# Kernel optimization log

Measured on AMD Instinct MI355X. Metric: run time of the kernel, lower is better.

Reference implementation:

```python
import jax, jax.numpy as jnp
import numpy as np

DIM = 1024
N_HEADS = 16
HEAD_DIM = DIM // N_HEADS
B, T = 2, 2048


def setup_inputs() -> dict:
    key = jax.random.key(0)
    ks = jax.random.split(key, 6)
    x = jax.random.normal(ks[0], (B, T, DIM), dtype=jnp.float32)
    # causal 0/1 mask, broadcastable over batch and heads
    mask = jnp.tril(jnp.ones((T, T), dtype=jnp.int32))[None, None, :, :]
    s = 1.0 / np.sqrt(DIM)
    W_qkv = jax.random.normal(ks[1], (DIM, 3 * DIM), dtype=jnp.float32) * s
    b_qkv = jnp.zeros((3 * DIM,), dtype=jnp.float32)
    W_proj = jax.random.normal(ks[2], (DIM, DIM), dtype=jnp.float32) * s
    b_proj = jnp.zeros((DIM,), dtype=jnp.float32)
    return {"x": x, "W_qkv": W_qkv, "b_qkv": b_qkv, "W_proj": W_proj, "b_proj": b_proj, "mask": mask}


def reference(x, W_qkv, b_qkv, W_proj, b_proj, mask):
    Bx, Tx, C = x.shape
    qkv = x @ W_qkv + b_qkv  # [B,T,3C]
    q, k, v = jnp.split(qkv, 3, axis=-1)
    # [B,T,C] -> [B,H,T,Dh]
    def split_heads(t):
        return t.reshape(Bx, Tx, N_HEADS, HEAD_DIM).transpose(0, 2, 1, 3)
    q, k, v = split_heads(q), split_heads(k), split_heads(v)
    att = jnp.einsum('bhqd,bhkd->bhqk', q, k) / jnp.sqrt(jnp.float32(HEAD_DIM))
    att = jnp.where(mask == 0, jnp.float32(-jnp.inf), att)
    att = jax.nn.softmax(att, axis=-1)
    # dropout is identity in eval mode
    out = jnp.einsum('bhqk,bhkd->bhqd', att, v)
    out = out.transpose(0, 2, 1, 3).reshape(Bx, Tx, C)
    return out @ W_proj + b_proj
```

## Files before the change

### kernel.cpp

```cpp
#include <hip/hip_runtime.h>
#include <hip/hip_bf16.h>
#include <stdint.h>

#define DIM   1024
#define NHEAD 16
#define HD    64
#define SEQ   2048
#define NTOK  4096
#define QKV_REGION (NTOK * DIM)

typedef short          bf16x8 __attribute__((ext_vector_type(8)));
typedef float          f32x4  __attribute__((ext_vector_type(4)));
typedef float          f32x16 __attribute__((ext_vector_type(16)));
typedef unsigned short u16x8  __attribute__((ext_vector_type(8)));
typedef unsigned short u16x4  __attribute__((ext_vector_type(4)));

__device__ __forceinline__ unsigned short f2bf(float f) {
  union { float f; unsigned u; } x; x.f = f;
  unsigned r = x.u + 0x7FFFu + ((x.u >> 16) & 1u);
  return (unsigned short)(r >> 16);
}

__device__ __forceinline__ unsigned pack2bf_tr(float a, float b) {
  union { float f; unsigned u; } x, y; x.f = a; y.f = b;
  return (x.u >> 16) | (y.u & 0xFFFF0000u);
}

__device__ __forceinline__ void gld16(void* lds, const void* g) {
  __builtin_amdgcn_global_load_lds(
      (const __attribute__((address_space(1))) unsigned int*)g,
      (__attribute__((address_space(3))) unsigned int*)lds, 16, 0, 0);
}

__global__ __launch_bounds__(256) void k_prep(const float* __restrict__ x,
                                              unsigned short* __restrict__ xb,
                                              const float* __restrict__ Wqkv,
                                              unsigned short* __restrict__ wqkvt,
                                              const float* __restrict__ Wproj,
                                              unsigned short* __restrict__ wprojt) {
  __shared__ unsigned short t[64][72];
  const int bid = blockIdx.x, tid = threadIdx.x;
  if (bid < 2048) {
    size_t i = ((size_t)bid * 256 + tid) * 8;
    float4 a = *(const float4*)(x + i);
    float4 b = *(const float4*)(x + i + 4);
    u16x8 o;
    o[0] = f2bf(a.x); o[1] = f2bf(a.y); o[2] = f2bf(a.z); o[3] = f2bf(a.w);
    o[4] = f2bf(b.x); o[5] = f2bf(b.y); o[6] = f2bf(b.z); o[7] = f2bf(b.w);
    *(u16x8*)(xb + i) = o;
    return;
  }
  const float* in; unsigned short* out; int C, bx, by;
  if (bid < 2816) { in = Wqkv; out = wqkvt; C = 3072; bx = (bid - 2048) % 48; by = (bid - 2048) / 48; }
  else            { in = Wproj; out = wprojt; C = 1024; bx = (bid - 2816) % 16; by = (bid - 2816) / 16; }
  const int R = 1024;
  int r0 = by * 64, c0 = bx * 64;
  int rr = tid >> 4, cc = (tid & 15) * 4;
#pragma unroll
  for (int p = 0; p < 4; p++) {
    int r = p * 16 + rr;
    float4 v = *(const float4*)(in + (size_t)(r0 + r) * C + c0 + cc);
    t[r][cc + 0] = f2bf(v.x); t[r][cc + 1] = f2bf(v.y);
    t[r][cc + 2] = f2bf(v.z); t[r][cc + 3] = f2bf(v.w);
  }
  __syncthreads();
#pragma unroll
  for (int p = 0; p < 4; p++) {
    int c = p * 16 + rr;
    u16x4 v;
    v[0] = t[cc + 0][c]; v[1] = t[cc + 1][c];
    v[2] = t[cc + 2][c]; v[3] = t[cc + 3][c];
    *(u16x4*)(out + (size_t)(c0 + c) * R + r0 + cc) = v;
  }
}

__global__ __launch_bounds__(256) void k_tr_v(const unsigned short* __restrict__ v,
                                              unsigned short* __restrict__ vt) {
  __shared__ unsigned short s[64][72];
  int bh = blockIdx.y, t0 = blockIdx.x * 64;
  const unsigned short* in = v + (size_t)bh * SEQ * HD + (size_t)t0 * HD;
  unsigned short* out = vt + (size_t)bh * HD * SEQ + t0;
  int tid = threadIdx.x;
  int rr = tid >> 3, cc = (tid & 7) * 8;
#pragma unroll
  for (int p = 0; p < 2; p++) {
    int r = p * 32 + rr;
    u16x8 x = *(const u16x8*)(in + r * HD + cc);
#pragma unroll
    for (int j = 0; j < 8; j++) s[r][cc + j] = x[j];
  }
  __syncthreads();
#pragma unroll
  for (int p = 0; p < 2; p++) {
    int d = p * 32 + rr;
    u16x8 o;
#pragma unroll
    for (int j = 0; j < 8; j++) o[j] = s[cc + j][d];
    *(u16x8*)(out + (size_t)d * SEQ + cc) = o;
  }
}

template <int EPI>
__global__ __launch_bounds__(256) void k_gemm_bt(const unsigned short* __restrict__ A,
                                                 const unsigned short* __restrict__ Bt,
                                                 const float* __restrict__ bias,
                                                 void* __restrict__ Cout,
                                                 int M, int N, int K) {
  __shared__ unsigned short Al[128 * 64];
  __shared__ unsigned short Bl[128 * 64];
  const int tid = threadIdx.x, lane = tid & 63, w = tid >> 6;
  const int wm = w >> 1, wn = w & 1;
  const int m0 = blockIdx.y * 128, n0 = blockIdx.x * 128;
  const int l31 = lane & 31, hl = lane >> 5;

  f32x16 acc[2][2];
#pragma unroll
  for (int mt = 0; mt < 2; mt++)
#pragma unroll
    for (int nt = 0; nt < 2; nt++)
#pragma unroll
      for (int r = 0; r < 16; r++) acc[mt][nt][r] = 0.f;

  for (int k0 = 0; k0 < K; k0 += 64) {
    __syncthreads();
#pragma unroll
    for (int i = 0; i < 4; i++) {
      int row = w * 32 + i * 8 + (lane >> 3);
      int ch = (lane & 7) ^ (row & 7);
      gld16(&Al[(w * 32 + i * 8) * 64], A + (size_t)(m0 + row) * K + k0 + ch * 8);
      gld16(&Bl[(w * 32 + i * 8) * 64], Bt + (size_t)(n0 + row) * K + k0 + ch * 8);
    }
    __syncthreads();
#pragma unroll
    for (int ks = 0; ks < 4; ks++) {
      bf16x8 af[2], bfr[2];
#pragma unroll
      for (int mt = 0; mt < 2; mt++) {
        int row = wm * 64 + mt * 32 + l31;
        int ch = (2 * ks + hl) ^ (row & 7);
        af[mt] = *(const bf16x8*)&Al[row * 64 + ch * 8];
      }
#pragma unroll
      for (int nt = 0; nt < 2; nt++) {
        int row = wn * 64 + nt * 32 + l31;
        int ch = (2 * ks + hl) ^ (row & 7);
        bfr[nt] = *(const bf16x8*)&Bl[row * 64 + ch * 8];
      }
#pragma unroll
      for (int mt = 0; mt < 2; mt++)
#pragma unroll
        for (int nt = 0; nt < 2; nt++)
          acc[mt][nt] = __builtin_amdgcn_mfma_f32_32x32x16_bf16(af[mt], bfr[nt], acc[mt][nt], 0, 0, 0);
    }
  }

#pragma unroll
  for (int mt = 0; mt < 2; mt++) {
#pragma unroll
    for (int nt = 0; nt < 2; nt++) {
      int col = n0 + wn * 64 + nt * 32 + l31;
      float bv = bias[col];
#pragma unroll
      for (int rg = 0; rg < 4; rg++)
#pragma unroll
        for (int ri = 0; ri < 4; ri++) {
          int row = m0 + wm * 64 + mt * 32 + ri + rg * 8 + hl * 4;
          float val = acc[mt][nt][rg * 4 + ri] + bv;
          if (EPI == 1) {
            ((float*)Cout)[(size_t)row * N + col] = val;
          } else {
            unsigned short* dst = (unsigned short*)Cout;
            int reg = col >> 10, nn = col & 1023;
            if (reg == 0) val *= 0.18033688011112042f;
            int h = nn >> 6, d = nn & 63;
            int b = row >> 11, t = row & 2047;
            size_t idx = (size_t)reg * QKV_REGION +
                         ((size_t)(b * NHEAD + h) * SEQ + t) * HD + d;
            dst[idx] = f2bf(val);
          }
        }
    }
  }
}

__global__ __launch_bounds__(512, 4) void k_attn(const unsigned short* __restrict__ Q,
                                                 const unsigned short* __restrict__ K,
                                                 const unsigned short* __restrict__ Vt,
                                                 unsigned short* __restrict__ O) {
  __shared__ unsigned short kl[2][2][64 * 64];
  __shared__ unsigned short vl[2][2][64 * 64];
  __shared__ float ml2[256];
  const int tid = threadIdx.x, lane = tid & 63, w = tid >> 6;
  const int hl = lane >> 5, q32 = lane & 31;
  const bool hb = (hl != 0);
  const int h = w >> 2, wr = w & 3;
  const int id = blockIdx.x;
  const int bh = id & 31;
  const int qt = (id < 256) ? (15 - (id >> 5)) : ((id >> 5) - 8);
  const unsigned short* Qb = Q + (size_t)bh * SEQ * HD;
  const unsigned short* Kb = K + (size_t)bh * SEQ * HD;
  const unsigned short* Vb = Vt + (size_t)bh * HD * SEQ;

  const int wq = qt * 128 + wr * 32;
  const int qmax = wq + 31;
  const int qg = wq + q32;
  const int nlo = qt + 1;
  const int kt0 = h ? nlo : 0;

  bf16x8 qf[4];
  {
    const unsigned short* qp = Qb + (size_t)(wq + q32) * HD + hl * 8;
#pragma unroll
    for (int ks = 0; ks < 4; ks++) qf[ks] = *(const bf16x8*)(qp + ks * 16);
  }

  f32x16 oacc[2];
#pragma unroll
  for (int nd = 0; nd < 2; nd++)
#pragma unroll
    for (int r = 0; r < 16; r++) oacc[nd][r] = 0.f;
  float mrun = -1e30f, lpart = 0.f;

#define ASTAGE(S, BUF)                                                                   \
  if ((S) < nlo) {                                                                       \
    const int kb_ = (kt0 + (S)) * 64;                                                    \
    _Pragma("unroll")                                                                    \
    for (int i = 0; i < 2; i++) {                                                        \
      int row = wr * 16 + i * 8 + (lane >> 3);                                           \
      int ch = (lane & 7) ^ (row & 7);                                                   \
      gld16(&kl[h][BUF][(wr * 16 + i * 8) * 64], Kb + (size_t)(kb_ + row) * HD + ch * 8);\
      gld16(&vl[h][BUF][(wr * 16 + i * 8) * 64], Vb + (size_t)row * SEQ + kb_ + ch * 8); \
    }                                                                                    \
  }

  ASTAGE(0, 0);
  __syncthreads();
  int cur = 0;

  for (int s = 0; s < nlo; s++) {
    ASTAGE(s + 1, cur ^ 1);
    const int kb = (kt0 + s) * 64;
    if (kb <= qmax) {
      f32x16 sacc[2];
#pragma unroll
      for (int nk = 0; nk < 2; nk++)
#pragma unroll
        for (int r = 0; r < 16; r++) sacc[nk][r] = 0.f;
      __builtin_amdgcn_s_setprio(1);
#pragma unroll
      for (int ks = 0; ks < 4; ks++) {
#pragma unroll
        for (int nk = 0; nk < 2; nk++) {
          int krow = nk * 32 + q32;
          int ch = (2 * ks + hl) ^ (krow & 7);
          bf16x8 kf = *(const bf16x8*)&kl[h][cur][krow * 64 + ch * 8];
          sacc[nk] = __builtin_amdgcn_mfma_f32_32x32x16_bf16(kf, qf[ks], sacc[nk], 0, 0, 0);
        }
      }
      __builtin_amdgcn_s_setprio(0);

      const bool nm = (kb + 63 > wq);
      if (nm) {
        const int kvbase = kb + hl * 4;
#pragma unroll
        for (int nk = 0; nk < 2; nk++)
#pragma unroll
          for (int rg = 0; rg < 4; rg++)
#pragma unroll
            for (int ri = 0; ri < 4; ri++) {
              int kv = kvbase + nk * 32 + rg * 8 + ri;
              if (kv > qg) sacc[nk][rg * 4 + ri] = -__builtin_inff();
            }
      }

      float tm[8];
#pragma unroll
      for (int i = 0; i < 8; i++)
        tm[i] = fmaxf(fmaxf(sacc[0][i], sacc[0][i + 8]),
                      fmaxf(sacc[1][i], sacc[1][i + 8]));
#pragma unroll
      for (int i = 0; i < 4; i++) tm[i] = fmaxf(tm[i], tm[i + 4]);
      float rmax = fmaxf(fmaxf(tm[0], tm[2]), fmaxf(tm[1], tm[3]));
      rmax = fmaxf(rmax, __shfl_xor(rmax, 32));

      if (!__all(rmax <= mrun + 8.0f)) {
        float mnew = fmaxf(mrun, rmax);
        float fac = exp2f(mrun - mnew);
        mrun = mnew;
        lpart *= fac;
#pragma unroll
        for (int rg = 0; rg < 4; rg++)
#pragma unroll
          for (int ri = 0; ri < 4; ri++) {
            float fr = __shfl(fac, ri + rg * 8 + hl * 4);
            oacc[0][rg * 4 + ri] *= fr;
            oacc[1][rg * 4 + ri] *= fr;
          }
      }

#pragma unroll
      for (int nk = 0; nk < 2; nk++)
#pragma unroll
        for (int r = 0; r < 16; r++)
          sacc[nk][r] = exp2f(sacc[nk][r] - mrun);
      {
        float ts[8];
#pragma unroll
        for (int i = 0; i < 8; i++)
          ts[i] = (sacc[0][i] + sacc[0][i + 8]) + (sacc[1][i] + sacc[1][i + 8]);
#pragma unroll
        for (int i = 0; i < 4; i++) ts[i] = ts[i] + ts[i + 4];
        lpart += (ts[0] + ts[2]) + (ts[1] + ts[3]);
      }

#pragma unroll
      for (int nk = 0; nk < 2; nk++) {
        unsigned cc[4][2];
#pragma unroll
        for (int m = 0; m < 4; m++) {
          cc[m][0] = pack2bf_tr(sacc[nk][4 * m + 0], sacc[nk][4 * m + 1]);
          cc[m][1] = pack2bf_tr(sacc[nk][4 * m + 2], sacc[nk][4 * m + 3]);
        }
        unsigned rv[2][2];
#pragma unroll
        for (int mm = 0; mm < 2; mm++) {
          unsigned sx = hb ? cc[2 * mm][0] : cc[2 * mm + 1][0];
          unsigned sy = hb ? cc[2 * mm][1] : cc[2 * mm + 1][1];
          rv[mm][0] = (unsigned)__shfl_xor((int)sx, 32);
          rv[mm][1] = (unsigned)__shfl_xor((int)sy, 32);
        }
        __builtin_amdgcn_s_setprio(1);
#pragma unroll
        for (int sl = 0; sl < 2; sl++) {
          const int me = 2 * sl;
          union { bf16x8 v; unsigned u[4]; } A;
          A.u[0] = hb ? rv[sl][0] : cc[me][0];
          A.u[1] = hb ? rv[sl][1] : cc[me][1];
          A.u[2] = hb ? cc[me + 1][0] : rv[sl][0];
          A.u[3] = hb ? cc[me + 1][1] : rv[sl][1];
          const int ss = nk * 2 + sl;
#pragma unroll
          for (int nd = 0; nd < 2; nd++) {
            int vrow = nd * 32 + q32;
            int ch = (2 * ss + hl) ^ (vrow & 7);
            bf16x8 vf = *(const bf16x8*)&vl[h][cur][vrow * 64 + ch * 8];
            oacc[nd] = __builtin_amdgcn_mfma_f32_32x32x16_bf16(A.v, vf, oacc[nd], 0, 0, 0);
          }
        }
        __builtin_amdgcn_s_setprio(0);
      }
    }
    __syncthreads();
    cur ^= 1;
  }
#undef ASTAGE

  float lf = lpart + __shfl_xor(lpart, 32);
  float* o1 = (float*)&kl[0][0][0];
  if (h == 1) {
#pragma unroll
    for (int nd = 0; nd < 2; nd++)
#pragma unroll
      for (int rg = 0; rg < 4; rg++)
#pragma unroll
        for (int ri = 0; ri < 4; ri++) {
          int row = wr * 32 + ri + rg * 8 + hl * 4;
          o1[row * 64 + nd * 32 + q32] = oacc[nd][rg * 4 + ri];
        }
    if (lane < 32) {
      ml2[(wr * 32 + lane) * 2 + 0] = mrun;
      ml2[(wr * 32 + lane) * 2 + 1] = lf;
    }
  }
  __syncthreads();
  if (h == 0) {
    const int b = bh >> 4, hh = bh & 15;
    float m1 = ml2[(wr * 32 + q32) * 2 + 0];
    float l1 = ml2[(wr * 32 + q32) * 2 + 1];
    float ms = fmaxf(mrun, m1);
    float f0 = exp2f(mrun - ms), f1 = exp2f(m1 - ms);
    float inv = 1.f / (lf * f0 + l1 * f1);
    float a0 = f0 * inv, a1 = f1 * inv;
#pragma unroll
    for (int rg = 0; rg < 4; rg++)
#pragma unroll
      for (int ri = 0; ri < 4; ri++) {
        int srcl = ri + rg * 8 + hl * 4;
        float b0 = __shfl(a0, srcl);
        float b1 = __shfl(a1, srcl);
        int row = wr * 32 + srcl;
        int t = qt * 128 + row;
#pragma unroll
        for (int nd = 0; nd < 2; nd++) {
          int d = nd * 32 + q32;
          float val = oacc[nd][rg * 4 + ri] * b0 + o1[row * 64 + d] * b1;
          O[((size_t)(b * SEQ + t)) * DIM + hh * HD + d] = f2bf(val);
        }
      }
  }
}

extern "C" void kernel_launch(void* const* d_in, const int* in_sizes, int n_in,
                              void* d_out, int out_size, void* d_ws, size_t ws_size,
                              hipStream_t stream) {
  const float* x     = (const float*)d_in[0];
  const float* Wqkv  = (const float*)d_in[1];
  const float* bqkv  = (const float*)d_in[2];
  const float* Wproj = (const float*)d_in[3];
  const float* bproj = (const float*)d_in[4];
  float* out = (float*)d_out;

  unsigned short* ws     = (unsigned short*)d_ws;
  unsigned short* xb_vt  = ws;
  unsigned short* wqkvt  = xb_vt + 4194304;
  unsigned short* wprojt = wqkvt + 3145728;
  unsigned short* q      = wprojt + 1048576;
  unsigned short* k      = q + 4194304;
  unsigned short* v_o    = k + 4194304;

  k_prep<<<3072, 256, 0, stream>>>(x, xb_vt, Wqkv, wqkvt, Wproj, wprojt);
  k_gemm_bt<0><<<dim3(24, 32), 256, 0, stream>>>(xb_vt, wqkvt, bqkv, q, NTOK, 3072, DIM);
  k_tr_v<<<dim3(32, 32), 256, 0, stream>>>(v_o, xb_vt);
  k_attn<<<dim3(512), 512, 0, stream>>>(q, k, xb_vt, v_o);
  k_gemm_bt<1><<<dim3(8, 32), 256, 0, stream>>>(v_o, wprojt, bproj, out, NTOK, DIM, DIM);
}
```

Measured before the change: 120.3 us.

## Add dedicated QKV GEMM kernel with 256x256 tiles and 4-stage async LDS pipeline

Splits the templated GEMM into a dedicated QKV projection kernel and a separate output-projection kernel. The QKV kernel uses 512-thread blocks computing 256x256 tiles with a 4-deep ring of LDS buffers filled by direct global-to-LDS loads and explicit vmcnt waits, so loads for upcoming K-slices overlap MFMA work on the current one. The larger tile raises arithmetic intensity, but the grid shrinks to 192 blocks, which may underfill the GPU's 256 CUs, and the kernel needs 128KB of LDS per block.

```diff
diff --git a/kernel.cpp b/kernel.cpp
--- a/kernel.cpp
+++ b/kernel.cpp
@@ -100,12 +100,114 @@
   }
 }
 
-template <int EPI>
-__global__ __launch_bounds__(256) void k_gemm_bt(const unsigned short* __restrict__ A,
-                                                 const unsigned short* __restrict__ Bt,
-                                                 const float* __restrict__ bias,
-                                                 void* __restrict__ Cout,
-                                                 int M, int N, int K) {
+__global__ __launch_bounds__(512, 2) void k_gemm_qkv(const unsigned short* __restrict__ A,
+                                                     const unsigned short* __restrict__ Bt,
+                                                     const float* __restrict__ bias,
+                                                     unsigned short* __restrict__ Cout,
+                                                     int M, int N, int K) {
+  __shared__ unsigned short lds[4][2][256 * 32];
+  const int tid = threadIdx.x, lane = tid & 63, w = tid >> 6;
+  const int wm = w >> 2, wn = w & 3;
+  const int l31 = lane & 31, hl = lane >> 5;
+  const int m0 = blockIdx.y * 256, n0 = blockIdx.x * 256;
+  const int NS = K >> 5;
+  const int csw = (tid & 3) ^ ((tid >> 2) & 3);
+
+  f32x16 acc[4][2];
+#pragma unroll
+  for (int mt = 0; mt < 4; mt++)
+#pragma unroll
+    for (int nt = 0; nt < 2; nt++)
+#pragma unroll
+      for (int r = 0; r < 16; r++) acc[mt][nt][r] = 0.f;
+
+#define QSTAGE(S)                                                                   \
+  if ((S) < NS) {                                                                   \
+    const int kk0 = (S) << 5;                                                       \
+    unsigned short* ab = &lds[(S) & 3][0][0];                                       \
+    unsigned short* bb = &lds[(S) & 3][1][0];                                       \
+    _Pragma("unroll")                                                               \
+    for (int i = 0; i < 2; i++) {                                                   \
+      int row = i * 128 + (tid >> 2);                                               \
+      gld16(ab + i * 4096 + tid * 8, A + (size_t)(m0 + row) * K + kk0 + csw * 8);   \
+      gld16(bb + i * 4096 + tid * 8, Bt + (size_t)(n0 + row) * K + kk0 + csw * 8);  \
+    }                                                                               \
+  }
+
+  QSTAGE(0); QSTAGE(1); QSTAGE(2);
+  asm volatile("s_waitcnt vmcnt(8)" ::: "memory");
+  __builtin_amdgcn_s_barrier();
+  __builtin_amdgcn_sched_barrier(0);
+
+  for (int s = 0; s < NS; s++) {
+    const unsigned short* ab = &lds[s & 3][0][0];
+    const unsigned short* bb = &lds[s & 3][1][0];
+
+#pragma unroll
+    for (int ks = 0; ks < 2; ks++) {
+      bf16x8 af[4], bfr[2];
+#pragma unroll
+      for (int mt = 0; mt < 4; mt++) {
+        int row = wm * 128 + mt * 32 + l31;
+        int ch = (ks * 2 + hl) ^ (l31 & 3);
+        af[mt] = *(const bf16x8*)&ab[row * 32 + ch * 8];
+      }
+#pragma unroll
+      for (int nt = 0; nt < 2; nt++) {
+        int row = wn * 64 + nt * 32 + l31;
+        int ch = (ks * 2 + hl) ^ (l31 & 3);
+        bfr[nt] = *(const bf16x8*)&bb[row * 32 + ch * 8];
+      }
+      __builtin_amdgcn_s_setprio(1);
+#pragma unroll
+      for (int mt = 0; mt < 4; mt++)
+#pragma unroll
+        for (int nt = 0; nt < 2; nt++)
+          acc[mt][nt] = __builtin_amdgcn_mfma_f32_32x32x16_bf16(af[mt], bfr[nt], acc[mt][nt], 0, 0, 0);
+      __builtin_amdgcn_s_setprio(0);
+    }
+
+    QSTAGE(s + 3);
+
+    if (s < NS - 1) {
+      if (s <= NS - 4)      asm volatile("s_waitcnt vmcnt(8)" ::: "memory");
+      else if (s == NS - 3) asm volatile("s_waitcnt vmcnt(4)" ::: "memory");
+      else                  asm volatile("s_waitcnt vmcnt(0)" ::: "memory");
+      __builtin_amdgcn_s_barrier();
+      __builtin_amdgcn_sched_barrier(0);
+    }
+  }
+#undef QSTAGE
+
+#pragma unroll
+  for (int mt = 0; mt < 4; mt++) {
+#pragma unroll
+    for (int nt = 0; nt < 2; nt++) {
+      int col = n0 + wn * 64 + nt * 32 + l31;
+      float bv = bias[col];
+#pragma unroll
+      for (int rg = 0; rg < 4; rg++)
+#pragma unroll
+        for (int ri = 0; ri < 4; ri++) {
+          int row = m0 + wm * 128 + mt * 32 + ri + rg * 8 + hl * 4;
+          float val = acc[mt][nt][rg * 4 + ri] + bv;
+          int reg = col >> 10, nn = col & 1023;
+          if (reg == 0) val *= 0.18033688011112042f;
+          int h = nn >> 6, d = nn & 63;
+          int b = row >> 11, t = row & 2047;
+          size_t idx = (size_t)reg * QKV_REGION +
+                       ((size_t)(b * NHEAD + h) * SEQ + t) * HD + d;
+          Cout[idx] = f2bf(val);
+        }
+    }
+  }
+}
+
+__global__ __launch_bounds__(256) void k_gemm_proj(const unsigned short* __restrict__ A,
+                                                   const unsigned short* __restrict__ Bt,
+                                                   const float* __restrict__ bias,
+                                                   float* __restrict__ Cout,
+                                                   int M, int N, int K) {
   __shared__ unsigned short Al[128 * 64];
   __shared__ unsigned short Bl[128 * 64];
   const int tid = threadIdx.x, lane = tid & 63, w = tid >> 6;
@@ -165,19 +267,7 @@
 #pragma unroll
         for (int ri = 0; ri < 4; ri++) {
           int row = m0 + wm * 64 + mt * 32 + ri + rg * 8 + hl * 4;
-          float val = acc[mt][nt][rg * 4 + ri] + bv;
-          if (EPI == 1) {
-            ((float*)Cout)[(size_t)row * N + col] = val;
-          } else {
-            unsigned short* dst = (unsigned short*)Cout;
-            int reg = col >> 10, nn = col & 1023;
-            if (reg == 0) val *= 0.18033688011112042f;
-            int h = nn >> 6, d = nn & 63;
-            int b = row >> 11, t = row & 2047;
-            size_t idx = (size_t)reg * QKV_REGION +
-                         ((size_t)(b * NHEAD + h) * SEQ + t) * HD + d;
-            dst[idx] = f2bf(val);
-          }
+          Cout[(size_t)row * N + col] = acc[mt][nt][rg * 4 + ri] + bv;
         }
     }
   }
@@ -333,18 +423,18 @@
 #pragma unroll
         for (int sl = 0; sl < 2; sl++) {
           const int me = 2 * sl;
-          union { bf16x8 v; unsigned u[4]; } A;
-          A.u[0] = hb ? rv[sl][0] : cc[me][0];
-          A.u[1] = hb ? rv[sl][1] : cc[me][1];
-          A.u[2] = hb ? cc[me + 1][0] : rv[sl][0];
-          A.u[3] = hb ? cc[me + 1][1] : rv[sl][1];
+          union { bf16x8 v; unsigned u[4]; } Afr;
+          Afr.u[0] = hb ? rv[sl][0] : cc[me][0];
+          Afr.u[1] = hb ? rv[sl][1] : cc[me][1];
+          Afr.u[2] = hb ? cc[me + 1][0] : rv[sl][0];
+          Afr.u[3] = hb ? cc[me + 1][1] : rv[sl][1];
           const int ss = nk * 2 + sl;
 #pragma unroll
           for (int nd = 0; nd < 2; nd++) {
             int vrow = nd * 32 + q32;
             int ch = (2 * ss + hl) ^ (vrow & 7);
             bf16x8 vf = *(const bf16x8*)&vl[h][cur][vrow * 64 + ch * 8];
-            oacc[nd] = __builtin_amdgcn_mfma_f32_32x32x16_bf16(A.v, vf, oacc[nd], 0, 0, 0);
+            oacc[nd] = __builtin_amdgcn_mfma_f32_32x32x16_bf16(Afr.v, vf, oacc[nd], 0, 0, 0);
           }
         }
         __builtin_amdgcn_s_setprio(0);
@@ -419,8 +509,8 @@
   unsigned short* v_o    = k + 4194304;
 
   k_prep<<<3072, 256, 0, stream>>>(x, xb_vt, Wqkv, wqkvt, Wproj, wprojt);
-  k_gemm_bt<0><<<dim3(24, 32), 256, 0, stream>>>(xb_vt, wqkvt, bqkv, q, NTOK, 3072, DIM);
+  k_gemm_qkv<<<dim3(12, 16), 512, 0, stream>>>(xb_vt, wqkvt, bqkv, q, NTOK, 3072, DIM);
   k_tr_v<<<dim3(32, 32), 256, 0, stream>>>(v_o, xb_vt);
   k_attn<<<dim3(512), 512, 0, stream>>>(q, k, xb_vt, v_o);
-  k_gemm_bt<1><<<dim3(8, 32), 256, 0, stream>>>(v_o, wprojt, bproj, out, NTOK, DIM, DIM);
-}
+  k_gemm_proj<<<dim3(8, 32), 256, 0, stream>>>(v_o, wprojt, bproj, out, NTOK, DIM, DIM);
+}
```

After: 125.5 us. 1.04x slower.
